# Performance work log

Measured on AMD Instinct MI355X. Metric: run time of the kernel, lower is better.

The kernel has to match this reference:

```python
import jax, jax.numpy as jnp
import numpy as np

EPS = 1e-5

def _layernorm(x, g, b):
    mu = jnp.mean(x, axis=-1, keepdims=True)
    var = jnp.mean(jnp.square(x - mu), axis=-1, keepdims=True)
    return (x - mu) * jax.lax.rsqrt(var + EPS) * g + b

def setup_inputs() -> dict:
    key = jax.random.key(0)
    ks = jax.random.split(key, 12)
    B, S, D, F = 2, 2048, 1024, 4096
    w = lambda k, shp: jax.random.normal(k, shp, dtype=jnp.float32) * 0.02
    return {
        "x":  jax.random.normal(ks[0], (B, S, D), dtype=jnp.float32),
        "Wq": w(ks[1], (D, D)), "bq": jnp.zeros((D,), jnp.float32),
        "Wk": w(ks[2], (D, D)), "bk": jnp.zeros((D,), jnp.float32),
        "Wv": w(ks[3], (D, D)), "bv": jnp.zeros((D,), jnp.float32),
        "W1": w(ks[4], (F, D)), "b1": jnp.zeros((F,), jnp.float32),
        "W2": w(ks[5], (D, F)), "b2": jnp.zeros((D,), jnp.float32),
        "g1": jnp.ones((D,), jnp.float32), "beta1": jnp.zeros((D,), jnp.float32),
        "g2": jnp.ones((D,), jnp.float32), "beta2": jnp.zeros((D,), jnp.float32),
    }

def reference(x, Wq, bq, Wk, bk, Wv, bv, W1, b1, W2, b2, g1, beta1, g2, beta2):
    B, S, D = x.shape
    H = 16
    dk = D // H
    # QKV projections (torch nn.Linear: y = x @ W.T + b)
    q = (x @ Wq.T + bq).reshape(B, S, H, dk).transpose(0, 2, 1, 3)  # [B,H,S,dk]
    k = (x @ Wk.T + bk).reshape(B, S, H, dk).transpose(0, 2, 1, 3)
    v = (x @ Wv.T + bv).reshape(B, S, H, dk).transpose(0, 2, 1, 3)
    # naive full attention (no mask, dropout=identity in eval)
    scores = jnp.einsum("bhqd,bhkd->bhqk", q, k) / jnp.sqrt(jnp.float32(dk))
    probs = jax.nn.softmax(scores, axis=-1)
    attn = jnp.einsum("bhqk,bhkd->bhqd", probs, v)  # [B,H,S,dk]
    attn_out = attn.transpose(0, 2, 1, 3).reshape(B, S, D)  # NOTE: no output proj (combine unused in source)
    # residual + LN1
    h = _layernorm(x + attn_out, g1, beta1)
    # FFN: linear2(relu(linear1(h)))
    ffn = jax.nn.relu(h @ W1.T + b1) @ W2.T + b2
    # residual + LN2
    return _layernorm(h + ffn, g2, beta2)
```

## Files before the change

kernel.cpp:

```cpp
#include <hip/hip_runtime.h>
#include <stdint.h>

typedef unsigned short u16;
typedef __bf16 bf16x8 __attribute__((ext_vector_type(8)));
typedef short s16x8 __attribute__((ext_vector_type(8)));
typedef float f32x4 __attribute__((ext_vector_type(4)));

union FragU { s16x8 s; bf16x8 b; uint4 u; };

__device__ __forceinline__ f32x4 mfma_bf16(s16x8 a, s16x8 b, f32x4 c) {
    FragU ua, ub; ua.s = a; ub.s = b;
    return __builtin_amdgcn_mfma_f32_16x16x32_bf16(ua.b, ub.b, c, 0, 0, 0);
}

__device__ __forceinline__ u16 f2bf(float f) {
    uint32_t u = __float_as_uint(f);
    u += 0x7fffu + ((u >> 16) & 1u);
    return (u16)(u >> 16);
}

__device__ __forceinline__ float bf2f(u16 u) {
    return __uint_as_float((uint32_t)u << 16);
}

__device__ __forceinline__ void gload_lds16(const void* g, void* l) {
    __builtin_amdgcn_global_load_lds((__attribute__((address_space(1))) void*)g,
                                     (__attribute__((address_space(3))) void*)l,
                                     16, 0, 0);
}

__device__ __forceinline__ void xcd_swz(int& bx, int& by, int& bz) {
    int nx = gridDim.x, ny = gridDim.y;
    int nwg = nx * ny * gridDim.z;
    int lin = blockIdx.x + nx * (blockIdx.y + ny * blockIdx.z);
    int cpx = nwg >> 3;
    int s = (lin & 7) * cpx + (lin >> 3);
    bx = s % nx; s /= nx;
    by = s % ny; bz = s / ny;
}

__global__ void k_cast(const float* __restrict__ in, u16* __restrict__ out, int n4) {
    int i = blockIdx.x * blockDim.x + threadIdx.x;
    int stride = gridDim.x * blockDim.x;
    for (; i < n4; i += stride) {
        float4 v = ((const float4*)in)[i];
        u16 us[4] = {f2bf(v.x), f2bf(v.y), f2bf(v.z), f2bf(v.w)};
        *(uint2*)(out + (size_t)i * 4) = *(uint2*)us;
    }
}

template<int RELU, int OUTMODE>
__device__ __forceinline__ void gemm_body(
    const u16* __restrict__ A, const u16* __restrict__ W,
    const float* __restrict__ bias, void* __restrict__ Cout,
    int M, int N, int K, int row0, int col0, int kbeg, int kend)
{
    __shared__ __align__(16) u16 As[128 * 64];
    __shared__ __align__(16) u16 Bs[128 * 64];

    const int tid  = threadIdx.x;
    const int wid  = tid >> 6;
    const int lane = tid & 63;
    const int g    = lane >> 4;
    const int cc   = lane & 15;
    const int wr   = wid >> 1;
    const int wc   = wid & 1;

    f32x4 zero = {0.f, 0.f, 0.f, 0.f};
    f32x4 acc[4][4];
#pragma unroll
    for (int i = 0; i < 4; i++)
#pragma unroll
        for (int j = 0; j < 4; j++) acc[i][j] = zero;

    const int srow = tid >> 3;
    const int scol = ((tid & 7) ^ (srow & 7)) * 8;
    const u16* gA0 = A + (size_t)(row0 + srow) * K + scol;
    const u16* gB0 = W + (size_t)(col0 + srow) * K + scol;
    u16* lA0 = &As[wid * 512];
    u16* lB0 = &Bs[wid * 512];

    const int xm = (cc & 7);

    for (int k0 = kbeg; k0 < kend; k0 += 64) {
#pragma unroll
        for (int j = 0; j < 4; j++)
            gload_lds16(gA0 + (size_t)(j * 32) * K + k0, lA0 + j * 2048);
#pragma unroll
        for (int j = 0; j < 4; j++)
            gload_lds16(gB0 + (size_t)(j * 32) * K + k0, lB0 + j * 2048);
        __syncthreads();

#pragma unroll
        for (int h = 0; h < 2; h++) {
            const int slot = ((h * 4 + g) ^ xm) * 8;
            s16x8 af[4], bf[4];
#pragma unroll
            for (int mi = 0; mi < 4; mi++)
                af[mi] = *(const s16x8*)&As[(wr * 64 + mi * 16 + cc) * 64 + slot];
#pragma unroll
            for (int ni = 0; ni < 4; ni++)
                bf[ni] = *(const s16x8*)&Bs[(wc * 64 + ni * 16 + cc) * 64 + slot];
#pragma unroll
            for (int mi = 0; mi < 4; mi++)
#pragma unroll
                for (int ni = 0; ni < 4; ni++)
                    acc[mi][ni] = mfma_bf16(af[mi], bf[ni], acc[mi][ni]);
        }
        __syncthreads();
    }

#pragma unroll
    for (int ni = 0; ni < 4; ni++) {
        int col = col0 + wc * 64 + ni * 16 + cc;
        float bvv = 0.f;
        if (OUTMODE != 2) bvv = bias[col];
#pragma unroll
        for (int mi = 0; mi < 4; mi++) {
            int row = row0 + wr * 64 + mi * 16 + g * 4;
#pragma unroll
            for (int r = 0; r < 4; r++) {
                float v = acc[mi][ni][r] + bvv;
                if (RELU) v = fmaxf(v, 0.f);
                size_t idx = (size_t)(row + r) * N + col;
                if (OUTMODE == 0) ((float*)Cout)[idx] = v;
                else              ((u16*)Cout)[idx] = f2bf(v);
            }
        }
    }
}

__global__ __launch_bounds__(256, 4) void k_gemm_qkv(
    const u16* __restrict__ A, const u16* __restrict__ Wq, const u16* __restrict__ Wk,
    const u16* __restrict__ Wv, const float* __restrict__ bq, const float* __restrict__ bk,
    const float* __restrict__ bv, u16* __restrict__ Q, u16* __restrict__ K,
    u16* __restrict__ V, int M, int N, int Kd)
{
    int bx, by, bz; xcd_swz(bx, by, bz);
    const u16* W; const float* bb; u16* out;
    if (bz == 0)      { W = Wq; bb = bq; out = Q; }
    else if (bz == 1) { W = Wk; bb = bk; out = K; }
    else              { W = Wv; bb = bv; out = V; }
    gemm_body<0, 1>(A, W, bb, out, M, N, Kd, by * 128, bx * 128, 0, Kd);
}

__global__ __launch_bounds__(256, 4) void k_gemm_relu_bf16(
    const u16* __restrict__ A, const u16* __restrict__ W, const float* __restrict__ bias,
    u16* __restrict__ C, int M, int N, int K)
{
    int bx, by, bz; xcd_swz(bx, by, bz);
    gemm_body<1, 1>(A, W, bias, C, M, N, K, by * 128, bx * 128, 0, K);
}

__global__ __launch_bounds__(256, 4) void k_gemm_part(
    const u16* __restrict__ A, const u16* __restrict__ W,
    u16* __restrict__ p0, u16* __restrict__ p1, u16* __restrict__ p2, u16* __restrict__ p3,
    int M, int N, int K)
{
    int bx, by, bz; xcd_swz(bx, by, bz);
    u16* out = (bz == 0) ? p0 : (bz == 1) ? p1 : (bz == 2) ? p2 : p3;
    gemm_body<0, 2>(A, W, nullptr, out, M, N, K, by * 128, bx * 128, bz * 1024, bz * 1024 + 1024);
}

__global__ __launch_bounds__(256) void k_transpose_v(const u16* __restrict__ V, u16* __restrict__ Vt)
{
    constexpr int S = 2048, Dm = 1024;
    __shared__ __align__(16) u16 tile[64][72];
    int s0 = blockIdx.x * 64;
    int h = blockIdx.y, b = blockIdx.z;
    int tid = threadIdx.x;
    int r = tid >> 2, ch = tid & 3;
    const u16* src = V + (size_t)(b * S + s0 + r) * Dm + h * 64;
    *(s16x8*)&tile[r][ch * 8]      = *(const s16x8*)(src + ch * 8);
    *(s16x8*)&tile[r][ch * 8 + 32] = *(const s16x8*)(src + ch * 8 + 32);
    __syncthreads();
    int dd = tid >> 2, kc = tid & 3;
    u16 tmp[16];
#pragma unroll
    for (int j = 0; j < 16; j++) tmp[j] = tile[kc * 16 + j][dd];
    u16* dst = Vt + ((size_t)(b * 16 + h) * 64 + dd) * S + s0 + kc * 16;
    *(s16x8*)dst       = *(const s16x8*)&tmp[0];
    *(s16x8*)(dst + 8) = *(const s16x8*)&tmp[8];
}

__global__ __launch_bounds__(512, 4) void k_flash(
    const u16* __restrict__ Q, const u16* __restrict__ Kb,
    const u16* __restrict__ Vt, float* __restrict__ O)
{
    constexpr int S = 2048, Dm = 1024, H = 16;
    constexpr int KVB = 128;
    constexpr float sc = 0.125f;
    int qt = blockIdx.x, h = blockIdx.y, b = blockIdx.z;
    int tid = threadIdx.x, wid = tid >> 6, lane = tid & 63;
    int g = lane >> 4, cc = lane & 15;

    __shared__ __align__(16) u16 Ks[128 * 64];
    __shared__ __align__(16) u16 Vs[64 * 128];

    int q0 = qt * 128 + wid * 16;
    size_t base = (size_t)b * S * Dm + h * 64;

    FragU uq0, uq1, qs0, qs1;
    uq0.s = *(const s16x8*)(Q + base + (size_t)(q0 + cc) * Dm + g * 8);
    uq1.s = *(const s16x8*)(Q + base + (size_t)(q0 + cc) * Dm + 32 + g * 8);
#pragma unroll
    for (int e = 0; e < 8; e++) {
        qs0.b[e] = (__bf16)((float)uq0.b[e] * sc);
        qs1.b[e] = (__bf16)((float)uq1.b[e] * sc);
    }
    s16x8 qf0 = qs0.s, qf1 = qs1.s;

    f32x4 zero = {0.f, 0.f, 0.f, 0.f};
    f32x4 o[4];
#pragma unroll
    for (int t = 0; t < 4; t++) o[t] = zero;
    float m_run = -1e30f, l_run = 0.f;

    const int krow = tid >> 3;
    const int kcol = ((tid & 7) ^ (krow & 7)) * 8;
    const u16* kSrcBase = Kb + base + (size_t)krow * Dm + kcol;
    u16* kDst0 = &Ks[wid * 512];
    u16* kDst1 = kDst0 + 4096;

    const int vrow = tid >> 3;
    const int vch  = (tid & 7) * 8;
    const int xmv  = (vrow & 7) << 3;
    const int cb0  = ((vch >> 5) << 5) | (((vch >> 4) & 1) << 2) | (((vch >> 2) & 3) << 3);
    const int cb1  = cb0 + 64;
    const u16* vSrcBase = Vt + (size_t)(b * H + h) * 64 * S + (size_t)vrow * S;
    u16* vq0a = &Vs[(vrow * 128 + cb0) ^ xmv];
    u16* vq0b = &Vs[(vrow * 128 + cb0 + 8) ^ xmv];
    u16* vq1a = &Vs[(vrow * 128 + cb1) ^ xmv];
    u16* vq1b = &Vs[(vrow * 128 + cb1 + 8) ^ xmv];

    s16x8 vpre0 = *(const s16x8*)(vSrcBase + vch);
    s16x8 vpre1 = *(const s16x8*)(vSrcBase + 64 + vch);

    const int xm = cc & 7;

    for (int kv0 = 0; kv0 < S; kv0 += KVB) {
        __syncthreads();
        gload_lds16(kSrcBase + (size_t)kv0 * Dm,        kDst0);
        gload_lds16(kSrcBase + (size_t)(kv0 + 64) * Dm, kDst1);
        {
            FragU a0, a1; a0.s = vpre0; a1.s = vpre1;
            *(uint2*)vq0a = make_uint2(a0.u.x, a0.u.y);
            *(uint2*)vq0b = make_uint2(a0.u.z, a0.u.w);
            *(uint2*)vq1a = make_uint2(a1.u.x, a1.u.y);
            *(uint2*)vq1b = make_uint2(a1.u.z, a1.u.w);
        }
        __syncthreads();
        if (kv0 + KVB < S) {
            vpre0 = *(const s16x8*)(vSrcBase + kv0 + KVB + vch);
            vpre1 = *(const s16x8*)(vSrcBase + kv0 + KVB + 64 + vch);
        }

        f32x4 sacc[8];
#pragma unroll
        for (int t = 0; t < 8; t++) sacc[t] = zero;
        __builtin_amdgcn_s_setprio(1);
#pragma unroll
        for (int t = 0; t < 8; t++) {
            const u16* kr = &Ks[(t * 16 + cc) * 64];
            s16x8 kf0 = *(const s16x8*)(kr + ((0 + g) ^ xm) * 8);
            s16x8 kf1 = *(const s16x8*)(kr + ((4 + g) ^ xm) * 8);
            sacc[t] = mfma_bf16(kf0, qf0, sacc[t]);
            sacc[t] = mfma_bf16(kf1, qf1, sacc[t]);
        }
        __builtin_amdgcn_s_setprio(0);

        float mx = fmaxf(fmaxf(sacc[0][0], sacc[0][1]), fmaxf(sacc[0][2], sacc[0][3]));
#pragma unroll
        for (int t = 1; t < 8; t++)
            mx = fmaxf(mx, fmaxf(fmaxf(sacc[t][0], sacc[t][1]), fmaxf(sacc[t][2], sacc[t][3])));
        mx = fmaxf(mx, __shfl_xor(mx, 16, 64));
        mx = fmaxf(mx, __shfl_xor(mx, 32, 64));

        if (!__all(mx - m_run <= 8.f)) {
            float mnew = fmaxf(m_run, mx);
            float a = __expf(m_run - mnew);
            l_run *= a;
#pragma unroll
            for (int t = 0; t < 4; t++)
#pragma unroll
                for (int i = 0; i < 4; i++) o[t][i] *= a;
            m_run = mnew;
        }

        float ssum = 0.f;
        FragU pb[4];
#pragma unroll
        for (int t = 0; t < 8; t++)
#pragma unroll
            for (int r = 0; r < 4; r++) {
                float pv = __expf(sacc[t][r] - m_run);
                ssum += pv;
                pb[t >> 1].b[(t & 1) * 4 + r] = (__bf16)pv;
            }
        ssum += __shfl_xor(ssum, 16, 64);
        ssum += __shfl_xor(ssum, 32, 64);
        l_run += ssum;

        __builtin_amdgcn_s_setprio(1);
#pragma unroll
        for (int td = 0; td < 4; td++) {
            const int rb = (td * 16 + cc) * 128;
#pragma unroll
            for (int kk = 0; kk < 4; kk++) {
                s16x8 vf = *(const s16x8*)&Vs[(rb + kk * 32 + g * 8) ^ (xm << 3)];
                o[td] = mfma_bf16(vf, pb[kk].s, o[td]);
            }
        }
        __builtin_amdgcn_s_setprio(0);
    }

    float inv = 1.f / l_run;
#pragma unroll
    for (int td = 0; td < 4; td++) {
        float4 st = {o[td][0] * inv, o[td][1] * inv, o[td][2] * inv, o[td][3] * inv};
        *(float4*)&O[(size_t)(b * S + q0 + cc) * Dm + h * 64 + td * 16 + g * 4] = st;
    }
}

template<int WRITE_BF>
__global__ __launch_bounds__(256) void k_ln(
    const float* __restrict__ A, const float* __restrict__ B,
    const float* __restrict__ gw, const float* __restrict__ bw,
    float* __restrict__ outf, u16* __restrict__ outb)
{
    constexpr int D = 1024;
    int row = blockIdx.x;
    int t = threadIdx.x;
    int lane = t & 63, wid = t >> 6;
    float4 va = ((const float4*)(A + (size_t)row * D))[t];
    float4 vb = ((const float4*)(B + (size_t)row * D))[t];
    float v0 = va.x + vb.x, v1 = va.y + vb.y, v2 = va.z + vb.z, v3 = va.w + vb.w;
    float sum = v0 + v1 + v2 + v3;
    float sq  = v0 * v0 + v1 * v1 + v2 * v2 + v3 * v3;
#pragma unroll
    for (int off = 1; off < 64; off <<= 1) {
        sum += __shfl_xor(sum, off, 64);
        sq  += __shfl_xor(sq,  off, 64);
    }
    __shared__ float s1[4], s2[4];
    if (lane == 0) { s1[wid] = sum; s2[wid] = sq; }
    __syncthreads();
    sum = s1[0] + s1[1] + s1[2] + s1[3];
    sq  = s2[0] + s2[1] + s2[2] + s2[3];
    float mu  = sum * (1.f / D);
    float var = sq * (1.f / D) - mu * mu;
    float rs  = rsqrtf(var + 1e-5f);
    float4 gv = ((const float4*)gw)[t];
    float4 bv = ((const float4*)bw)[t];
    float y0 = (v0 - mu) * rs * gv.x + bv.x;
    float y1 = (v1 - mu) * rs * gv.y + bv.y;
    float y2 = (v2 - mu) * rs * gv.z + bv.z;
    float y3 = (v3 - mu) * rs * gv.w + bv.w;
    float4 yo = {y0, y1, y2, y3};
    ((float4*)(outf + (size_t)row * D))[t] = yo;
    if (WRITE_BF) {
        u16 us[4] = {f2bf(y0), f2bf(y1), f2bf(y2), f2bf(y3)};
        *(uint2*)(outb + (size_t)row * D + t * 4) = *(uint2*)us;
    }
}

__global__ __launch_bounds__(256) void k_ln2(
    const float* __restrict__ A,
    const u16* __restrict__ p0, const u16* __restrict__ p1,
    const u16* __restrict__ p2, const u16* __restrict__ p3,
    const float* __restrict__ bias,
    const float* __restrict__ gw, const float* __restrict__ bw,
    float* __restrict__ outf)
{
    constexpr int D = 1024;
    int row = blockIdx.x;
    int t = threadIdx.x;
    int lane = t & 63, wid = t >> 6;
    size_t idx = (size_t)row * D + t * 4;
    float4 va = ((const float4*)(A + (size_t)row * D))[t];
    float4 bb = ((const float4*)bias)[t];
    float v0 = va.x + bb.x, v1 = va.y + bb.y, v2 = va.z + bb.z, v3 = va.w + bb.w;
    const u16* ps[4] = {p0, p1, p2, p3};
#pragma unroll
    for (int pi = 0; pi < 4; pi++) {
        uint2 q = *(const uint2*)(ps[pi] + idx);
        v0 += bf2f((u16)q.x);
        v1 += bf2f((u16)(q.x >> 16));
        v2 += bf2f((u16)q.y);
        v3 += bf2f((u16)(q.y >> 16));
    }
    float sum = v0 + v1 + v2 + v3;
    float sq  = v0 * v0 + v1 * v1 + v2 * v2 + v3 * v3;
#pragma unroll
    for (int off = 1; off < 64; off <<= 1) {
        sum += __shfl_xor(sum, off, 64);
        sq  += __shfl_xor(sq,  off, 64);
    }
    __shared__ float s1[4], s2[4];
    if (lane == 0) { s1[wid] = sum; s2[wid] = sq; }
    __syncthreads();
    sum = s1[0] + s1[1] + s1[2] + s1[3];
    sq  = s2[0] + s2[1] + s2[2] + s2[3];
    float mu  = sum * (1.f / D);
    float var = sq * (1.f / D) - mu * mu;
    float rs  = rsqrtf(var + 1e-5f);
    float4 gv = ((const float4*)gw)[t];
    float4 bv = ((const float4*)bw)[t];
    float4 yo = {(v0 - mu) * rs * gv.x + bv.x,
                 (v1 - mu) * rs * gv.y + bv.y,
                 (v2 - mu) * rs * gv.z + bv.z,
                 (v3 - mu) * rs * gv.w + bv.w};
    ((float4*)(outf + (size_t)row * D))[t] = yo;
}

extern "C" void kernel_launch(void* const* d_in, const int* in_sizes, int n_in,
                              void* d_out, int out_size, void* d_ws, size_t ws_size,
                              hipStream_t stream)
{
    constexpr int B = 2, S = 2048, D = 1024, F = 4096, H = 16;
    constexpr int M = B * S;
    const float* x   = (const float*)d_in[0];
    const float* Wq  = (const float*)d_in[1];
    const float* bq  = (const float*)d_in[2];
    const float* Wk  = (const float*)d_in[3];
    const float* bk  = (const float*)d_in[4];
    const float* Wv  = (const float*)d_in[5];
    const float* bv  = (const float*)d_in[6];
    const float* W1  = (const float*)d_in[7];
    const float* b1  = (const float*)d_in[8];
    const float* W2  = (const float*)d_in[9];
    const float* b2  = (const float*)d_in[10];
    const float* g1  = (const float*)d_in[11];
    const float* be1 = (const float*)d_in[12];
    const float* g2  = (const float*)d_in[13];
    const float* be2 = (const float*)d_in[14];
    float* out = (float*)d_out;

    char* ws = (char*)d_ws;
    size_t off = 0;
    auto alloc = [&](size_t bytes) {
        void* p = ws + off;
        off += (bytes + 255) & ~(size_t)255;
        return p;
    };
    u16* xb   = (u16*)alloc((size_t)M * D * 2);
    u16* wqb  = (u16*)alloc((size_t)D * D * 2);
    u16* wkb  = (u16*)alloc((size_t)D * D * 2);
    u16* wvb  = (u16*)alloc((size_t)D * D * 2);
    u16* w1b  = (u16*)alloc((size_t)F * D * 2);
    u16* w2b  = (u16*)alloc((size_t)D * F * 2);
    u16* Qb   = (u16*)alloc((size_t)M * D * 2);
    u16* Kbf  = (u16*)alloc((size_t)M * D * 2);
    u16* Vb   = (u16*)alloc((size_t)M * D * 2);
    u16* Vtb  = (u16*)alloc((size_t)M * D * 2);
    float* attn = (float*)alloc((size_t)M * D * 4);
    float* hf   = (float*)alloc((size_t)M * D * 4);
    u16* hb     = (u16*)alloc((size_t)M * D * 2);
    u16* ffn1   = Qb;
    u16* p0 = xb;
    u16* p1 = w1b;
    u16* p2 = (u16*)attn;
    u16* p3 = ((u16*)attn) + (size_t)M * D;

    dim3 blk(256);
    k_cast<<<dim3(512), blk, 0, stream>>>(x,  xb,  M * D / 4);
    k_cast<<<dim3(256), blk, 0, stream>>>(Wq, wqb, D * D / 4);
    k_cast<<<dim3(256), blk, 0, stream>>>(Wk, wkb, D * D / 4);
    k_cast<<<dim3(256), blk, 0, stream>>>(Wv, wvb, D * D / 4);
    k_cast<<<dim3(512), blk, 0, stream>>>(W1, w1b, F * D / 4);
    k_cast<<<dim3(512), blk, 0, stream>>>(W2, w2b, D * F / 4);

    k_gemm_qkv<<<dim3(D / 128, M / 128, 3), blk, 0, stream>>>(
        xb, wqb, wkb, wvb, bq, bk, bv, Qb, Kbf, Vb, M, D, D);
    k_transpose_v<<<dim3(S / 64, H, B), blk, 0, stream>>>(Vb, Vtb);
    k_flash<<<dim3(S / 128, H, B), dim3(512), 0, stream>>>(Qb, Kbf, Vtb, attn);
    k_ln<1><<<dim3(M), blk, 0, stream>>>(x, attn, g1, be1, hf, hb);
    k_gemm_relu_bf16<<<dim3(F / 128, M / 128), blk, 0, stream>>>(hb, w1b, b1, ffn1, M, F, D);
    k_gemm_part<<<dim3(D / 128, M / 128, 4), blk, 0, stream>>>(
        ffn1, w2b, p0, p1, p2, p3, M, D, F);
    k_ln2<<<dim3(M), blk, 0, stream>>>(hf, p0, p1, p2, p3, b2, g2, be2, out);
}
```

Before: 213.7 us.

## Double-buffer LDS tiles in GEMM and flash attention kernels

```diff
diff --git a/kernel.cpp b/kernel.cpp
--- a/kernel.cpp
+++ b/kernel.cpp
@@ -55,8 +55,8 @@
     const float* __restrict__ bias, void* __restrict__ Cout,
     int M, int N, int K, int row0, int col0, int kbeg, int kend)
 {
-    __shared__ __align__(16) u16 As[128 * 64];
-    __shared__ __align__(16) u16 Bs[128 * 64];
+    __shared__ __align__(16) u16 As[2][128 * 64];
+    __shared__ __align__(16) u16 Bs[2][128 * 64];
 
     const int tid  = threadIdx.x;
     const int wid  = tid >> 6;
@@ -77,35 +77,47 @@
     const int scol = ((tid & 7) ^ (srow & 7)) * 8;
     const u16* gA0 = A + (size_t)(row0 + srow) * K + scol;
     const u16* gB0 = W + (size_t)(col0 + srow) * K + scol;
-    u16* lA0 = &As[wid * 512];
-    u16* lB0 = &Bs[wid * 512];
 
     const int xm = (cc & 7);
 
-    for (int k0 = kbeg; k0 < kend; k0 += 64) {
+    auto stage = [&](int buf, int k0) {
+        u16* lA0 = &As[buf][wid * 512];
+        u16* lB0 = &Bs[buf][wid * 512];
 #pragma unroll
         for (int j = 0; j < 4; j++)
             gload_lds16(gA0 + (size_t)(j * 32) * K + k0, lA0 + j * 2048);
 #pragma unroll
         for (int j = 0; j < 4; j++)
             gload_lds16(gB0 + (size_t)(j * 32) * K + k0, lB0 + j * 2048);
-        __syncthreads();
-
+    };
+
+    stage(0, kbeg);
+    __syncthreads();
+
+    const int nsteps = (kend - kbeg) >> 6;
+    for (int step = 0; step < nsteps; ++step) {
+        const int cur = step & 1;
+        if (step + 1 < nsteps) stage(cur ^ 1, kbeg + (step + 1) * 64);
+
+        const u16* Asc = As[cur];
+        const u16* Bsc = Bs[cur];
 #pragma unroll
         for (int h = 0; h < 2; h++) {
             const int slot = ((h * 4 + g) ^ xm) * 8;
             s16x8 af[4], bf[4];
 #pragma unroll
             for (int mi = 0; mi < 4; mi++)
-                af[mi] = *(const s16x8*)&As[(wr * 64 + mi * 16 + cc) * 64 + slot];
+                af[mi] = *(const s16x8*)&Asc[(wr * 64 + mi * 16 + cc) * 64 + slot];
 #pragma unroll
             for (int ni = 0; ni < 4; ni++)
-                bf[ni] = *(const s16x8*)&Bs[(wc * 64 + ni * 16 + cc) * 64 + slot];
+                bf[ni] = *(const s16x8*)&Bsc[(wc * 64 + ni * 16 + cc) * 64 + slot];
+            __builtin_amdgcn_s_setprio(1);
 #pragma unroll
             for (int mi = 0; mi < 4; mi++)
 #pragma unroll
                 for (int ni = 0; ni < 4; ni++)
                     acc[mi][ni] = mfma_bf16(af[mi], bf[ni], acc[mi][ni]);
+            __builtin_amdgcn_s_setprio(0);
         }
         __syncthreads();
     }
@@ -130,7 +142,7 @@
     }
 }
 
-__global__ __launch_bounds__(256, 4) void k_gemm_qkv(
+__global__ __launch_bounds__(256, 2) void k_gemm_qkv(
     const u16* __restrict__ A, const u16* __restrict__ Wq, const u16* __restrict__ Wk,
     const u16* __restrict__ Wv, const float* __restrict__ bq, const float* __restrict__ bk,
     const float* __restrict__ bv, u16* __restrict__ Q, u16* __restrict__ K,
@@ -144,7 +156,7 @@
     gemm_body<0, 1>(A, W, bb, out, M, N, Kd, by * 128, bx * 128, 0, Kd);
 }
 
-__global__ __launch_bounds__(256, 4) void k_gemm_relu_bf16(
+__global__ __launch_bounds__(256, 2) void k_gemm_relu_bf16(
     const u16* __restrict__ A, const u16* __restrict__ W, const float* __restrict__ bias,
     u16* __restrict__ C, int M, int N, int K)
 {
@@ -152,7 +164,7 @@
     gemm_body<1, 1>(A, W, bias, C, M, N, K, by * 128, bx * 128, 0, K);
 }
 
-__global__ __launch_bounds__(256, 4) void k_gemm_part(
+__global__ __launch_bounds__(256, 2) void k_gemm_part(
     const u16* __restrict__ A, const u16* __restrict__ W,
     u16* __restrict__ p0, u16* __restrict__ p1, u16* __restrict__ p2, u16* __restrict__ p3,
     int M, int N, int K)
@@ -194,8 +206,8 @@
     int tid = threadIdx.x, wid = tid >> 6, lane = tid & 63;
     int g = lane >> 4, cc = lane & 15;
 
-    __shared__ __align__(16) u16 Ks[128 * 64];
-    __shared__ __align__(16) u16 Vs[64 * 128];
+    __shared__ __align__(16) u16 Ks[2][128 * 64];
+    __shared__ __align__(16) u16 Vs[2][64 * 128];
 
     int q0 = qt * 128 + wid * 16;
     size_t base = (size_t)b * S * Dm + h * 64;
@@ -219,8 +231,7 @@
     const int krow = tid >> 3;
     const int kcol = ((tid & 7) ^ (krow & 7)) * 8;
     const u16* kSrcBase = Kb + base + (size_t)krow * Dm + kcol;
-    u16* kDst0 = &Ks[wid * 512];
-    u16* kDst1 = kDst0 + 4096;
+    const int kDstOff = wid * 512;
 
     const int vrow = tid >> 3;
     const int vch  = (tid & 7) * 8;
@@ -228,40 +239,45 @@
     const int cb0  = ((vch >> 5) << 5) | (((vch >> 4) & 1) << 2) | (((vch >> 2) & 3) << 3);
     const int cb1  = cb0 + 64;
     const u16* vSrcBase = Vt + (size_t)(b * H + h) * 64 * S + (size_t)vrow * S;
-    u16* vq0a = &Vs[(vrow * 128 + cb0) ^ xmv];
-    u16* vq0b = &Vs[(vrow * 128 + cb0 + 8) ^ xmv];
-    u16* vq1a = &Vs[(vrow * 128 + cb1) ^ xmv];
-    u16* vq1b = &Vs[(vrow * 128 + cb1 + 8) ^ xmv];
-
-    s16x8 vpre0 = *(const s16x8*)(vSrcBase + vch);
-    s16x8 vpre1 = *(const s16x8*)(vSrcBase + 64 + vch);
+    const int vi0a = (vrow * 128 + cb0) ^ xmv;
+    const int vi0b = (vrow * 128 + cb0 + 8) ^ xmv;
+    const int vi1a = (vrow * 128 + cb1) ^ xmv;
+    const int vi1b = (vrow * 128 + cb1 + 8) ^ xmv;
 
     const int xm = cc & 7;
 
+    gload_lds16(kSrcBase,                   &Ks[0][kDstOff]);
+    gload_lds16(kSrcBase + (size_t)64 * Dm, &Ks[0][kDstOff + 4096]);
+    {
+        FragU a0, a1;
+        a0.s = *(const s16x8*)(vSrcBase + vch);
+        a1.s = *(const s16x8*)(vSrcBase + 64 + vch);
+        *(uint2*)&Vs[0][vi0a] = make_uint2(a0.u.x, a0.u.y);
+        *(uint2*)&Vs[0][vi0b] = make_uint2(a0.u.z, a0.u.w);
+        *(uint2*)&Vs[0][vi1a] = make_uint2(a1.u.x, a1.u.y);
+        *(uint2*)&Vs[0][vi1b] = make_uint2(a1.u.z, a1.u.w);
+    }
+    __syncthreads();
+
+    int cur = 0;
     for (int kv0 = 0; kv0 < S; kv0 += KVB) {
-        __syncthreads();
-        gload_lds16(kSrcBase + (size_t)kv0 * Dm,        kDst0);
-        gload_lds16(kSrcBase + (size_t)(kv0 + 64) * Dm, kDst1);
-        {
-            FragU a0, a1; a0.s = vpre0; a1.s = vpre1;
-            *(uint2*)vq0a = make_uint2(a0.u.x, a0.u.y);
-            *(uint2*)vq0b = make_uint2(a0.u.z, a0.u.w);
-            *(uint2*)vq1a = make_uint2(a1.u.x, a1.u.y);
-            *(uint2*)vq1b = make_uint2(a1.u.z, a1.u.w);
-        }
-        __syncthreads();
-        if (kv0 + KVB < S) {
+        const bool more = (kv0 + KVB < S);
+        s16x8 vpre0, vpre1;
+        if (more) {
+            gload_lds16(kSrcBase + (size_t)(kv0 + KVB) * Dm,      &Ks[cur ^ 1][kDstOff]);
+            gload_lds16(kSrcBase + (size_t)(kv0 + KVB + 64) * Dm, &Ks[cur ^ 1][kDstOff + 4096]);
             vpre0 = *(const s16x8*)(vSrcBase + kv0 + KVB + vch);
             vpre1 = *(const s16x8*)(vSrcBase + kv0 + KVB + 64 + vch);
         }
 
+        const u16* Kc = Ks[cur];
         f32x4 sacc[8];
 #pragma unroll
         for (int t = 0; t < 8; t++) sacc[t] = zero;
         __builtin_amdgcn_s_setprio(1);
 #pragma unroll
         for (int t = 0; t < 8; t++) {
-            const u16* kr = &Ks[(t * 16 + cc) * 64];
+            const u16* kr = &Kc[(t * 16 + cc) * 64];
             s16x8 kf0 = *(const s16x8*)(kr + ((0 + g) ^ xm) * 8);
             s16x8 kf1 = *(const s16x8*)(kr + ((4 + g) ^ xm) * 8);
             sacc[t] = mfma_bf16(kf0, qf0, sacc[t]);
@@ -301,17 +317,29 @@
         ssum += __shfl_xor(ssum, 32, 64);
         l_run += ssum;
 
+        const u16* Vc = Vs[cur];
         __builtin_amdgcn_s_setprio(1);
 #pragma unroll
         for (int td = 0; td < 4; td++) {
             const int rb = (td * 16 + cc) * 128;
 #pragma unroll
             for (int kk = 0; kk < 4; kk++) {
-                s16x8 vf = *(const s16x8*)&Vs[(rb + kk * 32 + g * 8) ^ (xm << 3)];
+                s16x8 vf = *(const s16x8*)&Vc[(rb + kk * 32 + g * 8) ^ (xm << 3)];
                 o[td] = mfma_bf16(vf, pb[kk].s, o[td]);
             }
         }
         __builtin_amdgcn_s_setprio(0);
+
+        if (more) {
+            FragU a0, a1; a0.s = vpre0; a1.s = vpre1;
+            u16* Vn = Vs[cur ^ 1];
+            *(uint2*)&Vn[vi0a] = make_uint2(a0.u.x, a0.u.y);
+            *(uint2*)&Vn[vi0b] = make_uint2(a0.u.z, a0.u.w);
+            *(uint2*)&Vn[vi1a] = make_uint2(a1.u.x, a1.u.y);
+            *(uint2*)&Vn[vi1b] = make_uint2(a1.u.z, a1.u.w);
+        }
+        __syncthreads();
+        cur ^= 1;
     }
 
     float inv = 1.f / l_run;
```

Result: slower. 231.0 us (+8.1%).
